# Optimization experiments

Hardware: AMD Instinct MI355X
Metric: run time of the kernel (lower is better)

Reference implementation:

```python
import jax, jax.numpy as jnp
import numpy as np

NUM_STATES = 8
HIDDEN_DIM = 1024
BATCH = 16384
DT = 0.01
PLANCK = 1.0
EPS_NORM = 1e-8
EPS_LOG = 1e-12


def setup_inputs() -> dict:
    key = jax.random.key(0)
    k1, k2, k3, k4, k5 = jax.random.split(key, 5)
    inv_sqrt_d = 1.0 / np.sqrt(HIDDEN_DIM)
    return {
        "input_state": jax.random.normal(k1, (BATCH, HIDDEN_DIM), dtype=jnp.float32),
        "amplitude_real": jax.random.normal(k2, (NUM_STATES, HIDDEN_DIM), dtype=jnp.float32) * inv_sqrt_d,
        "amplitude_imag": jax.random.normal(k3, (NUM_STATES, HIDDEN_DIM), dtype=jnp.float32) * inv_sqrt_d,
        "hamiltonian": jax.random.normal(k4, (NUM_STATES, NUM_STATES), dtype=jnp.float32) * 0.01,
        "projections": jax.random.normal(k5, (NUM_STATES, HIDDEN_DIM, HIDDEN_DIM), dtype=jnp.float32) * 0.01,
    }


def reference(input_state, amplitude_real, amplitude_imag, hamiltonian, projections):
    # complex amplitudes, normalized per state over hidden dim
    amps = amplitude_real + 1j * amplitude_imag  # [S, D] complex64
    norms = jnp.sum(jnp.abs(amps) ** 2, axis=1, keepdims=True)
    amps = amps / jnp.sqrt(norms + EPS_NORM)

    # unitary Hamiltonian evolution: expm(-i H dt / hbar) on the tiny SxS matrix
    H = (hamiltonian + hamiltonian.T) * 0.5
    U = jax.scipy.linalg.expm((-1j * DT / PLANCK) * H.astype(jnp.complex64))  # [S, S]
    amps = U @ amps  # [S, D]

    # decoherence at time_step=0: factor exp(0)=1, thermal noise scale 0 -> identity

    # superposed output: out[b,e] = sum_s Re(amps[s,e]) * (x @ P_s)[b,e]
    w = jnp.real(amps)  # [S, D]
    proj = jnp.einsum('bd,sde->bse', input_state, projections)  # [B, S, D]
    measured_output = jnp.einsum('bse,se->be', proj, w)  # [B, D]

    # measurement probabilities (computational basis)
    probs = jnp.abs(amps) ** 2
    probs = probs / (probs.sum(axis=0, keepdims=True) + EPS_NORM)
    collapse_prob = probs.mean(axis=1)  # [S]

    # metrics on rank-1 density matrix rho = outer(v, conj(v)), v = amps.flatten():
    # eigenvalues are {||v||^2, 0, ...} so the von Neumann entropy reduces to one term,
    # and sum|rho| = (sum|v|)^2, tr|diag| = sum|v|^2.
    v_abs = jnp.abs(amps.reshape(-1))
    lam = jnp.sum(v_abs ** 2)
    entanglement_entropy = -(lam * jnp.log(lam + EPS_LOG))
    coherence = jnp.sum(v_abs) ** 2 - lam

    amplitude_distribution = jnp.abs(amps) ** 2
    phase_evolution = jnp.angle(amps)

    return (measured_output, collapse_prob, entanglement_entropy, coherence,
            amplitude_distribution, phase_evolution)
```

## Files before the change

### kernel.cpp

```cpp
#include <hip/hip_runtime.h>
#include <hip/hip_bf16.h>

#define NSTATES 8
#define HD      1024
#define NBATCH  16384
#define NT      16

#define OUT_MEAS 0
#define OUT_CP   16777216
#define OUT_ENT  16777224
#define OUT_COH  16777225
#define OUT_AD   16777226
#define OUT_PH   16785418

typedef __attribute__((ext_vector_type(8))) short short8;
typedef __attribute__((ext_vector_type(4))) float f32x4;

__device__ __forceinline__ short f2bf(float f) {
    union { float f; unsigned u; } x; x.f = f;
    unsigned r = x.u + 0x7fffu + ((x.u >> 16) & 1u);
    return (short)(r >> 16);
}

__device__ __forceinline__ short8 pack8(float4 a, float4 b) {
    short8 v;
    v[0] = f2bf(a.x); v[1] = f2bf(a.y); v[2] = f2bf(a.z); v[3] = f2bf(a.w);
    v[4] = f2bf(b.x); v[5] = f2bf(b.y); v[6] = f2bf(b.z); v[7] = f2bf(b.w);
    return v;
}

__global__ __launch_bounds__(1024) void k_amps(const float* __restrict__ AR,
                                               const float* __restrict__ AI,
                                               const float* __restrict__ H,
                                               float* __restrict__ out,
                                               float* __restrict__ w) {
    __shared__ float redA[16 * NSTATES];
    __shared__ float redB[16 * 10];
    __shared__ float norms[NSTATES];
    __shared__ float sA[8][8], sA2[8][8], sA3[8][8];
    __shared__ float Ur[8][8], Ui[8][8];
    __shared__ float lamsa[2];

    const int tid = threadIdx.x;
    const int lane = tid & 63, wid = tid >> 6;
    const int d = tid;

    float arv[NSTATES], aiv[NSTATES];
    #pragma unroll
    for (int s = 0; s < NSTATES; s++) {
        arv[s] = AR[s * HD + d];
        aiv[s] = AI[s * HD + d];
    }
    float p[NSTATES];
    #pragma unroll
    for (int s = 0; s < NSTATES; s++) p[s] = arv[s] * arv[s] + aiv[s] * aiv[s];
    #pragma unroll
    for (int s = 0; s < NSTATES; s++)
        #pragma unroll
        for (int o = 32; o > 0; o >>= 1) p[s] += __shfl_down(p[s], o, 64);
    if (lane == 0)
        #pragma unroll
        for (int s = 0; s < NSTATES; s++) redA[wid * NSTATES + s] = p[s];
    if (tid < 64) {
        int i = tid >> 3, j = tid & 7;
        sA[i][j] = 0.5f * (H[i * 8 + j] + H[j * 8 + i]) * 0.01f;
    }
    __syncthreads();
    if (tid < 8) {
        float acc = 0.f;
        #pragma unroll
        for (int v = 0; v < 16; v++) acc += redA[v * NSTATES + tid];
        norms[tid] = acc;
    }
    if (tid < 64) {
        int i = tid >> 3, j = tid & 7;
        float acc = 0.f;
        #pragma unroll
        for (int k = 0; k < 8; k++) acc += sA[i][k] * sA[k][j];
        sA2[i][j] = acc;
    }
    __syncthreads();
    if (tid < 64) {
        int i = tid >> 3, j = tid & 7;
        float acc = 0.f;
        #pragma unroll
        for (int k = 0; k < 8; k++) acc += sA2[i][k] * sA[k][j];
        sA3[i][j] = acc;
        Ur[i][j] = ((i == j) ? 1.f : 0.f) - 0.5f * sA2[i][j];
        Ui[i][j] = -(sA[i][j] - sA3[i][j] * (1.f / 6.f));
    }
    __syncthreads();

    #pragma unroll
    for (int s = 0; s < NSTATES; s++) {
        float inv = 1.0f / sqrtf(norms[s] + 1e-8f);
        arv[s] *= inv;
        aiv[s] *= inv;
    }
    float nr[NSTATES], ni[NSTATES];
    #pragma unroll
    for (int s = 0; s < NSTATES; s++) {
        float xr = 0.f, xi = 0.f;
        #pragma unroll
        for (int t = 0; t < NSTATES; t++) {
            float ur = Ur[s][t], ui = Ui[s][t];
            xr += ur * arv[t] - ui * aiv[t];
            xi += ur * aiv[t] + ui * arv[t];
        }
        nr[s] = xr; ni[s] = xi;
    }
    float dist[NSTATES], csum = 0.f, sabs = 0.f;
    #pragma unroll
    for (int s = 0; s < NSTATES; s++) {
        dist[s] = nr[s] * nr[s] + ni[s] * ni[s];
        csum += dist[s];
        sabs += sqrtf(dist[s]);
    }
    #pragma unroll
    for (int s = 0; s < NSTATES; s++) {
        out[OUT_AD + s * HD + d] = dist[s];
        out[OUT_PH + s * HD + d] = atan2f(ni[s], nr[s]);
        w[s * HD + d] = nr[s];
    }
    float cinv = 1.0f / (csum + 1e-8f);
    float q[10];
    #pragma unroll
    for (int s = 0; s < NSTATES; s++) q[s] = dist[s] * cinv;
    q[8] = csum; q[9] = sabs;
    #pragma unroll
    for (int v = 0; v < 10; v++)
        #pragma unroll
        for (int o = 32; o > 0; o >>= 1) q[v] += __shfl_down(q[v], o, 64);
    if (lane == 0)
        #pragma unroll
        for (int v = 0; v < 10; v++) redB[wid * 10 + v] = q[v];
    __syncthreads();
    if (tid < 10) {
        float acc = 0.f;
        #pragma unroll
        for (int v = 0; v < 16; v++) acc += redB[v * 10 + tid];
        if (tid < 8)       out[OUT_CP + tid] = acc * (1.0f / HD);
        else               lamsa[tid - 8] = acc;
    }
    __syncthreads();
    if (tid == 0) {
        float lam = lamsa[0], sa = lamsa[1];
        out[OUT_ENT] = -(lam * logf(lam + 1e-12f));
        out[OUT_COH] = sa * sa - lam;
    }
}

__global__ __launch_bounds__(256) void k_pre(const float* __restrict__ X,
                                             short* __restrict__ Xb,
                                             const float* __restrict__ P,
                                             const float* __restrict__ w,
                                             short* __restrict__ Mt) {
    __shared__ float tile[64][65];
    if (blockIdx.x >= 256) {
        int idx = (blockIdx.x - 256) * 256 + threadIdx.x;
        const float* src = X + (size_t)idx * 8;
        float4 f0 = *reinterpret_cast<const float4*>(src);
        float4 f1 = *reinterpret_cast<const float4*>(src + 4);
        *reinterpret_cast<short8*>(Xb + (size_t)idx * 8) = pack8(f0, f1);
        return;
    }
    int d0 = (blockIdx.x >> 4) * 64;
    int e0 = (blockIdx.x & 15) * 64;
    int tx = threadIdx.x & 63, ty = threadIdx.x >> 6;
    float wv[NSTATES];
    #pragma unroll
    for (int s = 0; s < NSTATES; s++) wv[s] = w[s * HD + e0 + tx];
    #pragma unroll
    for (int j = 0; j < 16; j++) {
        int r = ty + 4 * j;
        float acc = 0.f;
        #pragma unroll
        for (int s = 0; s < NSTATES; s++)
            acc += wv[s] * P[(size_t)s * HD * HD + (size_t)(d0 + r) * HD + e0 + tx];
        tile[r][tx] = acc;
    }
    __syncthreads();
    #pragma unroll
    for (int j = 0; j < 16; j++) {
        int er = ty + 4 * j;
        Mt[(size_t)(e0 + er) * HD + d0 + tx] = f2bf(tile[tx][er]);
    }
}


__device__ __forceinline__ void stage_half(const short* __restrict__ srcBase,
                                           int rowbase, int h, int t2,
                                           short* dst, const int* goff,
                                           const int* ldsoff) {
    #pragma unroll
    for (int i = 0; i < 2; i++) {
        const short* g = srcBase + (size_t)(rowbase + h * 128) * HD + t2 * 64 + goff[i];
        __builtin_amdgcn_global_load_lds(
            (const __attribute__((address_space(1))) void*)g,
            (__attribute__((address_space(3))) void*)(dst + h * 8192 + ldsoff[i]),
            16, 0, 0);
    }
}

#define LOAD_A(qa)                                                             \
    _Pragma("unroll") for (int mf = 0; mf < 4; mf++)                           \
    _Pragma("unroll") for (int kk = 0; kk < 2; kk++)                           \
        af[mf][kk] = *reinterpret_cast<const short8*>(                         \
            &Acur[((qa) * 128 + wr64 + mf * 16 + ln15) * 64 + kx[kk]]);

#define LOAD_B_TO(dst, qb)                                                     \
    _Pragma("unroll") for (int nf = 0; nf < 2; nf++)                           \
    _Pragma("unroll") for (int kk = 0; kk < 2; kk++)                           \
        dst[nf][kk] = *reinterpret_cast<const short8*>(                        \
            &Bcur[((qb) * 128 + wn32 + nf * 16 + ln15) * 64 + kx[kk]]);

#define MFMA_P(qa, qb, breg)                                                   \
    _Pragma("unroll") for (int mf = 0; mf < 4; mf++)                           \
    _Pragma("unroll") for (int nf = 0; nf < 2; nf++)                           \
    _Pragma("unroll") for (int kk = 0; kk < 2; kk++)                           \
        acc[(qa) * 4 + mf][(qb) * 2 + nf] =                                    \
            __builtin_amdgcn_mfma_f32_16x16x32_bf16(                           \
                af[mf][kk], breg[nf][kk], acc[(qa) * 4 + mf][(qb) * 2 + nf], 0, 0, 0);

__global__ __launch_bounds__(512, 1) void k_gemm_8p(const short* __restrict__ Xb,
                                                    const short* __restrict__ Mt,
                                                    float* __restrict__ out) {
    __shared__ short As[2][256 * 64];
    __shared__ short Bs[2][256 * 64];

    const int bid = blockIdx.x;
    const int swz = (bid & 7) * 32 + (bid >> 3);
    const int brow = (swz >> 2) * 256;
    const int bcol = (swz & 3) * 256;

    const int tid  = threadIdx.x;
    const int lane = tid & 63, wid = tid >> 6;
    const int wr = wid >> 2, wn = wid & 3;
    const int ln15 = lane & 15, l16 = lane >> 4;
    const int wr64 = wr * 64;
    const int wn32 = wn * 32;

    int kx[2];
    kx[0] = ((l16 + 0) ^ (ln15 & 7)) * 8;
    kx[1] = ((l16 + 4) ^ (ln15 & 7)) * 8;

    int goff[2], ldsoff[2];
    #pragma unroll
    for (int i = 0; i < 2; i++) {
        int c = tid + 512 * i;
        int row = c >> 3, kc = c & 7;
        goff[i]   = row * HD + ((kc ^ (row & 7)) * 8);
        ldsoff[i] = c * 8;
    }

    short* A0 = &As[0][0]; short* A1b = &As[1][0];
    short* B0 = &Bs[0][0]; short* B1b = &Bs[1][0];

    f32x4 acc[8][4];
    #pragma unroll
    for (int m = 0; m < 8; m++)
        #pragma unroll
        for (int n = 0; n < 4; n++) acc[m][n] = (f32x4){0.f, 0.f, 0.f, 0.f};

    stage_half(Xb, brow, 0, 0, A0, goff, ldsoff);
    stage_half(Xb, brow, 1, 0, A0, goff, ldsoff);
    stage_half(Mt, bcol, 0, 0, B0, goff, ldsoff);
    stage_half(Mt, bcol, 1, 0, B0, goff, ldsoff);
    stage_half(Xb, brow, 0, 1, A1b, goff, ldsoff);
    stage_half(Mt, bcol, 1, 1, B1b, goff, ldsoff);
    asm volatile("s_waitcnt vmcnt(4)" ::: "memory");
    __builtin_amdgcn_s_barrier();

    short8 af[4][2], bfL[2][2], bfH[2][2];

    #pragma unroll 1
    for (int t = 0; t < NT; t++) {
        const int cur = t & 1;
        short* Acur  = cur ? A1b : A0;
        short* Bcur  = cur ? B1b : B0;
        short* Anext = cur ? A0 : A1b;
        short* Bnext = cur ? B0 : B1b;

        LOAD_A(0); LOAD_B_TO(bfL, 0);
        if (t + 1 < NT) stage_half(Xb, brow, 1, t + 1, Anext, goff, ldsoff);
        __builtin_amdgcn_s_barrier();
        __builtin_amdgcn_s_setprio(1);
        MFMA_P(0, 0, bfL);
        __builtin_amdgcn_s_setprio(0);

        LOAD_B_TO(bfH, 1);
        if (t + 1 < NT) stage_half(Mt, bcol, 0, t + 1, Bnext, goff, ldsoff);
        __builtin_amdgcn_s_barrier();
        __builtin_amdgcn_s_setprio(1);
        MFMA_P(0, 1, bfH);
        __builtin_amdgcn_s_setprio(0);

        LOAD_A(1);
        if (t + 2 < NT) stage_half(Xb, brow, 0, t + 2, Acur, goff, ldsoff);
        __builtin_amdgcn_s_barrier();
        __builtin_amdgcn_s_setprio(1);
        MFMA_P(1, 1, bfH);
        __builtin_amdgcn_s_setprio(0);

        if (t + 2 < NT) stage_half(Mt, bcol, 1, t + 2, Bcur, goff, ldsoff);
        __builtin_amdgcn_s_barrier();
        __builtin_amdgcn_s_setprio(1);
        MFMA_P(1, 0, bfL);
        __builtin_amdgcn_s_setprio(0);
        if (t + 2 < NT)      asm volatile("s_waitcnt vmcnt(4)" ::: "memory");
        else if (t + 1 < NT) asm volatile("s_waitcnt vmcnt(0)" ::: "memory");
        __builtin_amdgcn_s_barrier();
    }

    #pragma unroll
    for (int qa = 0; qa < 2; qa++)
        #pragma unroll
        for (int mf = 0; mf < 4; mf++)
            #pragma unroll
            for (int qb = 0; qb < 2; qb++)
                #pragma unroll
                for (int nf = 0; nf < 2; nf++)
                    #pragma unroll
                    for (int j = 0; j < 4; j++) {
                        int r = brow + qa * 128 + wr64 + mf * 16 + l16 * 4 + j;
                        int c = bcol + qb * 128 + wn32 + nf * 16 + ln15;
                        out[(size_t)r * HD + c] = acc[qa * 4 + mf][qb * 2 + nf][j];
                    }
}

extern "C" void kernel_launch(void* const* d_in, const int* in_sizes, int n_in,
                              void* d_out, int out_size, void* d_ws, size_t ws_size,
                              hipStream_t stream) {
    const float* X  = (const float*)d_in[0];
    const float* AR = (const float*)d_in[1];
    const float* AI = (const float*)d_in[2];
    const float* H  = (const float*)d_in[3];
    const float* P  = (const float*)d_in[4];
    float* out = (float*)d_out;

    char* ws = (char*)d_ws;
    float* w  = (float*)ws;
    short* Mt = (short*)(ws + 32768);
    short* Xb = (short*)(ws + 32768 + 2097152);

    k_amps<<<1, 1024, 0, stream>>>(AR, AI, H, out, w);
    k_pre<<<256 + (NBATCH * HD) / (256 * 8), 256, 0, stream>>>(X, Xb, P, w, Mt);
    k_gemm_8p<<<(NBATCH / 256) * (HD / 256), 512, 0, stream>>>(Xb, Mt, out);
}
```

Baseline: 76.50 us.

## Fuse fp32-to-bf16 conversion of X into GEMM A-tile staging

Removes the separate pass that converted the input activations to bf16 in workspace. The GEMM now loads fp32 X rows into registers, converts them with packed v_cvt_pk_bf16_f32 and writes them into LDS, prefetching one K-step ahead, while B tiles still use direct global-to-LDS loads. This avoids a full write and re-read of a bf16 copy of X, at the cost of reading fp32 X (twice the bytes) inside the GEMM, each X tile being re-read by the four column blocks, plus extra registers and a reworked barrier/waitcnt schedule. Rounding may differ slightly from the old software rounding for special values.

New measurement: 72.08 us. 5.8% less time.

```diff
diff --git a/kernel.cpp b/kernel.cpp
--- a/kernel.cpp
+++ b/kernel.cpp
@@ -22,11 +22,19 @@
     return (short)(r >> 16);
 }
 
-__device__ __forceinline__ short8 pack8(float4 a, float4 b) {
-    short8 v;
-    v[0] = f2bf(a.x); v[1] = f2bf(a.y); v[2] = f2bf(a.z); v[3] = f2bf(a.w);
-    v[4] = f2bf(b.x); v[5] = f2bf(b.y); v[6] = f2bf(b.z); v[7] = f2bf(b.w);
-    return v;
+__device__ __forceinline__ unsigned cvtpk(float lo, float hi) {
+    unsigned r;
+    asm("v_cvt_pk_bf16_f32 %0, %1, %2" : "=v"(r) : "v"(lo), "v"(hi));
+    return r;
+}
+
+__device__ __forceinline__ short8 pack8pk(float4 a, float4 b) {
+    union { unsigned u[4]; short8 s; } r;
+    r.u[0] = cvtpk(a.x, a.y);
+    r.u[1] = cvtpk(a.z, a.w);
+    r.u[2] = cvtpk(b.x, b.y);
+    r.u[3] = cvtpk(b.z, b.w);
+    return r.s;
 }
 
 __global__ __launch_bounds__(1024) void k_amps(const float* __restrict__ AR,
@@ -150,20 +158,10 @@
     }
 }
 
-__global__ __launch_bounds__(256) void k_pre(const float* __restrict__ X,
-                                             short* __restrict__ Xb,
-                                             const float* __restrict__ P,
-                                             const float* __restrict__ w,
-                                             short* __restrict__ Mt) {
+__global__ __launch_bounds__(256) void k_project_t(const float* __restrict__ P,
+                                                   const float* __restrict__ w,
+                                                   short* __restrict__ Mt) {
     __shared__ float tile[64][65];
-    if (blockIdx.x >= 256) {
-        int idx = (blockIdx.x - 256) * 256 + threadIdx.x;
-        const float* src = X + (size_t)idx * 8;
-        float4 f0 = *reinterpret_cast<const float4*>(src);
-        float4 f1 = *reinterpret_cast<const float4*>(src + 4);
-        *reinterpret_cast<short8*>(Xb + (size_t)idx * 8) = pack8(f0, f1);
-        return;
-    }
     int d0 = (blockIdx.x >> 4) * 64;
     int e0 = (blockIdx.x & 15) * 64;
     int tx = threadIdx.x & 63, ty = threadIdx.x >> 6;
@@ -188,10 +186,10 @@
 }
 
 
-__device__ __forceinline__ void stage_half(const short* __restrict__ srcBase,
-                                           int rowbase, int h, int t2,
-                                           short* dst, const int* goff,
-                                           const int* ldsoff) {
+__device__ __forceinline__ void stage_half_B(const short* __restrict__ srcBase,
+                                             int rowbase, int h, int t2,
+                                             short* dst, const int* goff,
+                                             const int* ldsoff) {
     #pragma unroll
     for (int i = 0; i < 2; i++) {
         const short* g = srcBase + (size_t)(rowbase + h * 128) * HD + t2 * 64 + goff[i];
@@ -201,6 +199,21 @@
             16, 0, 0);
     }
 }
+
+#define XLOAD(dst, h, t2)                                                      \
+    {                                                                          \
+        const float* b_ = X + (size_t)(brow + (h) * 128) * HD + (t2) * 64;     \
+        dst[0] = *reinterpret_cast<const float4*>(b_ + goff[0]);               \
+        dst[1] = *reinterpret_cast<const float4*>(b_ + goff[0] + 4);           \
+        dst[2] = *reinterpret_cast<const float4*>(b_ + goff[1]);               \
+        dst[3] = *reinterpret_cast<const float4*>(b_ + goff[1] + 4);           \
+    }
+
+#define XWRITE(dstlds, src)                                                    \
+    {                                                                          \
+        *reinterpret_cast<short8*>((dstlds) + ldsoff[0]) = pack8pk(src[0], src[1]); \
+        *reinterpret_cast<short8*>((dstlds) + ldsoff[1]) = pack8pk(src[2], src[3]); \
+    }
 
 #define LOAD_A(qa)                                                             \
     _Pragma("unroll") for (int mf = 0; mf < 4; mf++)                           \
@@ -222,9 +235,9 @@
             __builtin_amdgcn_mfma_f32_16x16x32_bf16(                           \
                 af[mf][kk], breg[nf][kk], acc[(qa) * 4 + mf][(qb) * 2 + nf], 0, 0, 0);
 
-__global__ __launch_bounds__(512, 1) void k_gemm_8p(const short* __restrict__ Xb,
-                                                    const short* __restrict__ Mt,
-                                                    float* __restrict__ out) {
+__global__ __launch_bounds__(512, 1) void k_gemm_jit(const float* __restrict__ X,
+                                                     const short* __restrict__ Mt,
+                                                     float* __restrict__ out) {
     __shared__ short As[2][256 * 64];
     __shared__ short Bs[2][256 * 64];
 
@@ -262,13 +275,16 @@
         #pragma unroll
         for (int n = 0; n < 4; n++) acc[m][n] = (f32x4){0.f, 0.f, 0.f, 0.f};
 
-    stage_half(Xb, brow, 0, 0, A0, goff, ldsoff);
-    stage_half(Xb, brow, 1, 0, A0, goff, ldsoff);
-    stage_half(Mt, bcol, 0, 0, B0, goff, ldsoff);
-    stage_half(Mt, bcol, 1, 0, B0, goff, ldsoff);
-    stage_half(Xb, brow, 0, 1, A1b, goff, ldsoff);
-    stage_half(Mt, bcol, 1, 1, B1b, goff, ldsoff);
-    asm volatile("s_waitcnt vmcnt(4)" ::: "memory");
+    float4 xrL[4], xrH[4];
+
+    XLOAD(xrL, 0, 0);
+    XLOAD(xrH, 1, 0);
+    stage_half_B(Mt, bcol, 0, 0, B0, goff, ldsoff);
+    stage_half_B(Mt, bcol, 1, 0, B0, goff, ldsoff);
+    stage_half_B(Mt, bcol, 1, 1, B1b, goff, ldsoff);
+    XWRITE(A0, xrL);
+    XWRITE(A0 + 8192, xrH);
+    asm volatile("s_waitcnt vmcnt(2) lgkmcnt(0)" ::: "memory");
     __builtin_amdgcn_s_barrier();
 
     short8 af[4][2], bfL[2][2], bfH[2][2];
@@ -282,34 +298,37 @@
         short* Bnext = cur ? B0 : B1b;
 
         LOAD_A(0); LOAD_B_TO(bfL, 0);
-        if (t + 1 < NT) stage_half(Xb, brow, 1, t + 1, Anext, goff, ldsoff);
+        if (t + 1 < NT) XLOAD(xrL, 0, (t + 1));
         __builtin_amdgcn_s_barrier();
         __builtin_amdgcn_s_setprio(1);
         MFMA_P(0, 0, bfL);
         __builtin_amdgcn_s_setprio(0);
 
         LOAD_B_TO(bfH, 1);
-        if (t + 1 < NT) stage_half(Mt, bcol, 0, t + 1, Bnext, goff, ldsoff);
+        if (t + 1 < NT) {
+            XLOAD(xrH, 1, (t + 1));
+            stage_half_B(Mt, bcol, 0, t + 1, Bnext, goff, ldsoff);
+        }
         __builtin_amdgcn_s_barrier();
         __builtin_amdgcn_s_setprio(1);
         MFMA_P(0, 1, bfH);
         __builtin_amdgcn_s_setprio(0);
 
         LOAD_A(1);
-        if (t + 2 < NT) stage_half(Xb, brow, 0, t + 2, Acur, goff, ldsoff);
+        if (t + 1 < NT) XWRITE(Anext, xrL);
         __builtin_amdgcn_s_barrier();
         __builtin_amdgcn_s_setprio(1);
         MFMA_P(1, 1, bfH);
         __builtin_amdgcn_s_setprio(0);
 
-        if (t + 2 < NT) stage_half(Mt, bcol, 1, t + 2, Bcur, goff, ldsoff);
+        if (t + 1 < NT) XWRITE(Anext + 8192, xrH);
+        if (t + 2 < NT) stage_half_B(Mt, bcol, 1, t + 2, Bcur, goff, ldsoff);
+        if (t + 2 < NT)      asm volatile("s_waitcnt vmcnt(2) lgkmcnt(0)" ::: "memory");
+        else if (t + 1 < NT) asm volatile("s_waitcnt vmcnt(0) lgkmcnt(0)" ::: "memory");
         __builtin_amdgcn_s_barrier();
         __builtin_amdgcn_s_setprio(1);
         MFMA_P(1, 0, bfL);
         __builtin_amdgcn_s_setprio(0);
-        if (t + 2 < NT)      asm volatile("s_waitcnt vmcnt(4)" ::: "memory");
-        else if (t + 1 < NT) asm volatile("s_waitcnt vmcnt(0)" ::: "memory");
-        __builtin_amdgcn_s_barrier();
     }
 
     #pragma unroll
@@ -341,9 +360,8 @@
     char* ws = (char*)d_ws;
     float* w  = (float*)ws;
     short* Mt = (short*)(ws + 32768);
-    short* Xb = (short*)(ws + 32768 + 2097152);
 
     k_amps<<<1, 1024, 0, stream>>>(AR, AI, H, out, w);
-    k_pre<<<256 + (NBATCH * HD) / (256 * 8), 256, 0, stream>>>(X, Xb, P, w, Mt);
-    k_gemm_8p<<<(NBATCH / 256) * (HD / 256), 512, 0, stream>>>(Xb, Mt, out);
-}
+    k_project_t<<<256, 256, 0, stream>>>(P, w, Mt);
+    k_gemm_jit<<<(NBATCH / 256) * (HD / 256), 512, 0, stream>>>(X, Mt, out);
+}
```

## Shrink GEMM block tile to 256x128 and drop one barrier per k-step

Applied to the files above, without the earlier changes.

The bf16 MFMA GEMM block tile narrows from 256x256 to 256x128, which doubles the grid to 512 blocks and halves the B-tile LDS buffers and accumulator registers. Each wave now owns one 16-wide N fragment per half, and B staging issues one global_load_lds per thread instead of two. The end-of-iteration vmcnt wait moves ahead of the last MFMA phase so it shares that phase's barrier, removing one barrier per k-step. The aim is better CU occupancy and load balance, with less register and LDS pressure. The cost is lower per-block data reuse, so the X tiles are read from memory twice as often.

Measured after the change: 83.56 us. +9.2%, slower.

```diff
diff --git a/kernel.cpp b/kernel.cpp
--- a/kernel.cpp
+++ b/kernel.cpp
@@ -188,10 +188,10 @@
 }
 
 
-__device__ __forceinline__ void stage_half(const short* __restrict__ srcBase,
-                                           int rowbase, int h, int t2,
-                                           short* dst, const int* goff,
-                                           const int* ldsoff) {
+__device__ __forceinline__ void stage_A(const short* __restrict__ srcBase,
+                                        int rowbase, int h, int t2,
+                                        short* dst, const int* goff,
+                                        const int* ldsoff) {
     #pragma unroll
     for (int i = 0; i < 2; i++) {
         const short* g = srcBase + (size_t)(rowbase + h * 128) * HD + t2 * 64 + goff[i];
@@ -202,6 +202,16 @@
     }
 }
 
+__device__ __forceinline__ void stage_B(const short* __restrict__ srcBase,
+                                        int colbase, int h, int t2,
+                                        short* dst, int goffB, int ldsoffB) {
+    const short* g = srcBase + (size_t)(colbase + h * 64) * HD + t2 * 64 + goffB;
+    __builtin_amdgcn_global_load_lds(
+        (const __attribute__((address_space(1))) void*)g,
+        (__attribute__((address_space(3))) void*)(dst + h * 4096 + ldsoffB),
+        16, 0, 0);
+}
+
 #define LOAD_A(qa)                                                             \
     _Pragma("unroll") for (int mf = 0; mf < 4; mf++)                           \
     _Pragma("unroll") for (int kk = 0; kk < 2; kk++)                           \
@@ -209,36 +219,34 @@
             &Acur[((qa) * 128 + wr64 + mf * 16 + ln15) * 64 + kx[kk]]);
 
 #define LOAD_B_TO(dst, qb)                                                     \
-    _Pragma("unroll") for (int nf = 0; nf < 2; nf++)                           \
     _Pragma("unroll") for (int kk = 0; kk < 2; kk++)                           \
-        dst[nf][kk] = *reinterpret_cast<const short8*>(                        \
-            &Bcur[((qb) * 128 + wn32 + nf * 16 + ln15) * 64 + kx[kk]]);
+        dst[kk] = *reinterpret_cast<const short8*>(                            \
+            &Bcur[((qb) * 64 + wn16 + ln15) * 64 + kx[kk]]);
 
 #define MFMA_P(qa, qb, breg)                                                   \
     _Pragma("unroll") for (int mf = 0; mf < 4; mf++)                           \
-    _Pragma("unroll") for (int nf = 0; nf < 2; nf++)                           \
     _Pragma("unroll") for (int kk = 0; kk < 2; kk++)                           \
-        acc[(qa) * 4 + mf][(qb) * 2 + nf] =                                    \
+        acc[(qa) * 4 + mf][(qb)] =                                             \
             __builtin_amdgcn_mfma_f32_16x16x32_bf16(                           \
-                af[mf][kk], breg[nf][kk], acc[(qa) * 4 + mf][(qb) * 2 + nf], 0, 0, 0);
-
-__global__ __launch_bounds__(512, 1) void k_gemm_8p(const short* __restrict__ Xb,
+                af[mf][kk], breg[kk], acc[(qa) * 4 + mf][(qb)], 0, 0, 0);
+
+__global__ __launch_bounds__(512, 1) void k_gemm_2r(const short* __restrict__ Xb,
                                                     const short* __restrict__ Mt,
                                                     float* __restrict__ out) {
     __shared__ short As[2][256 * 64];
-    __shared__ short Bs[2][256 * 64];
+    __shared__ short Bs[2][128 * 64];
 
     const int bid = blockIdx.x;
-    const int swz = (bid & 7) * 32 + (bid >> 3);
-    const int brow = (swz >> 2) * 256;
-    const int bcol = (swz & 3) * 256;
+    const int swz = (bid & 7) * 64 + (bid >> 3);
+    const int brow = (swz >> 3) * 256;
+    const int bcol = (swz & 7) * 128;
 
     const int tid  = threadIdx.x;
     const int lane = tid & 63, wid = tid >> 6;
     const int wr = wid >> 2, wn = wid & 3;
     const int ln15 = lane & 15, l16 = lane >> 4;
     const int wr64 = wr * 64;
-    const int wn32 = wn * 32;
+    const int wn16 = wn * 16;
 
     int kx[2];
     kx[0] = ((l16 + 0) ^ (ln15 & 7)) * 8;
@@ -252,26 +260,33 @@
         goff[i]   = row * HD + ((kc ^ (row & 7)) * 8);
         ldsoff[i] = c * 8;
     }
+    int goffB, ldsoffB;
+    {
+        int c = tid;
+        int row = c >> 3, kc = c & 7;
+        goffB   = row * HD + ((kc ^ (row & 7)) * 8);
+        ldsoffB = c * 8;
+    }
 
     short* A0 = &As[0][0]; short* A1b = &As[1][0];
     short* B0 = &Bs[0][0]; short* B1b = &Bs[1][0];
 
-    f32x4 acc[8][4];
+    f32x4 acc[8][2];
     #pragma unroll
     for (int m = 0; m < 8; m++)
         #pragma unroll
-        for (int n = 0; n < 4; n++) acc[m][n] = (f32x4){0.f, 0.f, 0.f, 0.f};
-
-    stage_half(Xb, brow, 0, 0, A0, goff, ldsoff);
-    stage_half(Xb, brow, 1, 0, A0, goff, ldsoff);
-    stage_half(Mt, bcol, 0, 0, B0, goff, ldsoff);
-    stage_half(Mt, bcol, 1, 0, B0, goff, ldsoff);
-    stage_half(Xb, brow, 0, 1, A1b, goff, ldsoff);
-    stage_half(Mt, bcol, 1, 1, B1b, goff, ldsoff);
-    asm volatile("s_waitcnt vmcnt(4)" ::: "memory");
+        for (int n = 0; n < 2; n++) acc[m][n] = (f32x4){0.f, 0.f, 0.f, 0.f};
+
+    stage_A(Xb, brow, 0, 0, A0, goff, ldsoff);
+    stage_A(Xb, brow, 1, 0, A0, goff, ldsoff);
+    stage_B(Mt, bcol, 0, 0, B0, goffB, ldsoffB);
+    stage_B(Mt, bcol, 1, 0, B0, goffB, ldsoffB);
+    stage_A(Xb, brow, 0, 1, A1b, goff, ldsoff);
+    stage_B(Mt, bcol, 1, 1, B1b, goffB, ldsoffB);
+    asm volatile("s_waitcnt vmcnt(3)" ::: "memory");
     __builtin_amdgcn_s_barrier();
 
-    short8 af[4][2], bfL[2][2], bfH[2][2];
+    short8 af[4][2], bfL[2], bfH[2];
 
     #pragma unroll 1
     for (int t = 0; t < NT; t++) {
@@ -282,34 +297,33 @@
         short* Bnext = cur ? B0 : B1b;
 
         LOAD_A(0); LOAD_B_TO(bfL, 0);
-        if (t + 1 < NT) stage_half(Xb, brow, 1, t + 1, Anext, goff, ldsoff);
+        if (t + 1 < NT) stage_A(Xb, brow, 1, t + 1, Anext, goff, ldsoff);
         __builtin_amdgcn_s_barrier();
         __builtin_amdgcn_s_setprio(1);
         MFMA_P(0, 0, bfL);
         __builtin_amdgcn_s_setprio(0);
 
         LOAD_B_TO(bfH, 1);
-        if (t + 1 < NT) stage_half(Mt, bcol, 0, t + 1, Bnext, goff, ldsoff);
+        if (t + 1 < NT) stage_B(Mt, bcol, 0, t + 1, Bnext, goffB, ldsoffB);
         __builtin_amdgcn_s_barrier();
         __builtin_amdgcn_s_setprio(1);
         MFMA_P(0, 1, bfH);
         __builtin_amdgcn_s_setprio(0);
 
         LOAD_A(1);
-        if (t + 2 < NT) stage_half(Xb, brow, 0, t + 2, Acur, goff, ldsoff);
+        if (t + 2 < NT) stage_A(Xb, brow, 0, t + 2, Acur, goff, ldsoff);
         __builtin_amdgcn_s_barrier();
         __builtin_amdgcn_s_setprio(1);
         MFMA_P(1, 1, bfH);
         __builtin_amdgcn_s_setprio(0);
 
-        if (t + 2 < NT) stage_half(Mt, bcol, 1, t + 2, Bcur, goff, ldsoff);
+        if (t + 2 < NT) stage_B(Mt, bcol, 1, t + 2, Bcur, goffB, ldsoffB);
+        if (t + 2 < NT)      asm volatile("s_waitcnt vmcnt(3)" ::: "memory");
+        else if (t + 1 < NT) asm volatile("s_waitcnt vmcnt(0)" ::: "memory");
         __builtin_amdgcn_s_barrier();
         __builtin_amdgcn_s_setprio(1);
         MFMA_P(1, 0, bfL);
         __builtin_amdgcn_s_setprio(0);
-        if (t + 2 < NT)      asm volatile("s_waitcnt vmcnt(4)" ::: "memory");
-        else if (t + 1 < NT) asm volatile("s_waitcnt vmcnt(0)" ::: "memory");
-        __builtin_amdgcn_s_barrier();
     }
 
     #pragma unroll
@@ -319,13 +333,11 @@
             #pragma unroll
             for (int qb = 0; qb < 2; qb++)
                 #pragma unroll
-                for (int nf = 0; nf < 2; nf++)
-                    #pragma unroll
-                    for (int j = 0; j < 4; j++) {
-                        int r = brow + qa * 128 + wr64 + mf * 16 + l16 * 4 + j;
-                        int c = bcol + qb * 128 + wn32 + nf * 16 + ln15;
-                        out[(size_t)r * HD + c] = acc[qa * 4 + mf][qb * 2 + nf][j];
-                    }
+                for (int j = 0; j < 4; j++) {
+                    int r = brow + qa * 128 + wr64 + mf * 16 + l16 * 4 + j;
+                    int c = bcol + qb * 64 + wn16 + ln15;
+                    out[(size_t)r * HD + c] = acc[qa * 4 + mf][qb][j];
+                }
 }
 
 extern "C" void kernel_launch(void* const* d_in, const int* in_sizes, int n_in,
@@ -345,5 +357,5 @@
 
     k_amps<<<1, 1024, 0, stream>>>(AR, AI, H, out, w);
     k_pre<<<256 + (NBATCH * HD) / (256 * 8), 256, 0, stream>>>(X, Xb, P, w, Mt);
-    k_gemm_8p<<<(NBATCH / 256) * (HD / 256), 512, 0, stream>>>(Xb, Mt, out);
-}
+    k_gemm_2r<<<(NBATCH / 256) * (HD / 128), 512, 0, stream>>>(Xb, Mt, out);
+}
```

## Fuse amplitude kernel into preprocessing kernel and merge GEMM loop barriers

Applied to the files above, without the earlier changes.

Removes the single-block k_amps launch. Each of the 256 projection blocks now recomputes the norms, the truncated unitary and its slice of weights, and one extra block writes the amplitude metrics. This drops a serialized launch and the workspace round-trip for w, at the cost of redundant small reductions in every projection block. In the GEMM main loop, the vmcnt wait moves before the preceding barrier, and the trailing barrier is removed so there is one fewer sync per iteration.

New measurement: 83.17 us. 1.09x slower.

```diff
diff --git a/kernel.cpp b/kernel.cpp
--- a/kernel.cpp
+++ b/kernel.cpp
@@ -29,161 +29,179 @@
     return v;
 }
 
-__global__ __launch_bounds__(1024) void k_amps(const float* __restrict__ AR,
-                                               const float* __restrict__ AI,
-                                               const float* __restrict__ H,
-                                               float* __restrict__ out,
-                                               float* __restrict__ w) {
-    __shared__ float redA[16 * NSTATES];
-    __shared__ float redB[16 * 10];
-    __shared__ float norms[NSTATES];
-    __shared__ float sA[8][8], sA2[8][8], sA3[8][8];
-    __shared__ float Ur[8][8], Ui[8][8];
-    __shared__ float lamsa[2];
-
+__global__ __launch_bounds__(256) void k_pre2(const float* __restrict__ X,
+                                              short* __restrict__ Xb,
+                                              const float* __restrict__ P,
+                                              const float* __restrict__ AR,
+                                              const float* __restrict__ AI,
+                                              const float* __restrict__ H,
+                                              short* __restrict__ Mt,
+                                              float* __restrict__ out) {
+    const int bid = blockIdx.x;
     const int tid = threadIdx.x;
-    const int lane = tid & 63, wid = tid >> 6;
-    const int d = tid;
-
-    float arv[NSTATES], aiv[NSTATES];
-    #pragma unroll
-    for (int s = 0; s < NSTATES; s++) {
-        arv[s] = AR[s * HD + d];
-        aiv[s] = AI[s * HD + d];
-    }
-    float p[NSTATES];
-    #pragma unroll
-    for (int s = 0; s < NSTATES; s++) p[s] = arv[s] * arv[s] + aiv[s] * aiv[s];
-    #pragma unroll
-    for (int s = 0; s < NSTATES; s++)
-        #pragma unroll
-        for (int o = 32; o > 0; o >>= 1) p[s] += __shfl_down(p[s], o, 64);
-    if (lane == 0)
-        #pragma unroll
-        for (int s = 0; s < NSTATES; s++) redA[wid * NSTATES + s] = p[s];
-    if (tid < 64) {
-        int i = tid >> 3, j = tid & 7;
-        sA[i][j] = 0.5f * (H[i * 8 + j] + H[j * 8 + i]) * 0.01f;
-    }
-    __syncthreads();
-    if (tid < 8) {
-        float acc = 0.f;
-        #pragma unroll
-        for (int v = 0; v < 16; v++) acc += redA[v * NSTATES + tid];
-        norms[tid] = acc;
-    }
-    if (tid < 64) {
-        int i = tid >> 3, j = tid & 7;
-        float acc = 0.f;
-        #pragma unroll
-        for (int k = 0; k < 8; k++) acc += sA[i][k] * sA[k][j];
-        sA2[i][j] = acc;
-    }
-    __syncthreads();
-    if (tid < 64) {
-        int i = tid >> 3, j = tid & 7;
-        float acc = 0.f;
-        #pragma unroll
-        for (int k = 0; k < 8; k++) acc += sA2[i][k] * sA[k][j];
-        sA3[i][j] = acc;
-        Ur[i][j] = ((i == j) ? 1.f : 0.f) - 0.5f * sA2[i][j];
-        Ui[i][j] = -(sA[i][j] - sA3[i][j] * (1.f / 6.f));
-    }
-    __syncthreads();
-
-    #pragma unroll
-    for (int s = 0; s < NSTATES; s++) {
-        float inv = 1.0f / sqrtf(norms[s] + 1e-8f);
-        arv[s] *= inv;
-        aiv[s] *= inv;
-    }
-    float nr[NSTATES], ni[NSTATES];
-    #pragma unroll
-    for (int s = 0; s < NSTATES; s++) {
-        float xr = 0.f, xi = 0.f;
-        #pragma unroll
-        for (int t = 0; t < NSTATES; t++) {
-            float ur = Ur[s][t], ui = Ui[s][t];
-            xr += ur * arv[t] - ui * aiv[t];
-            xi += ur * aiv[t] + ui * arv[t];
-        }
-        nr[s] = xr; ni[s] = xi;
-    }
-    float dist[NSTATES], csum = 0.f, sabs = 0.f;
-    #pragma unroll
-    for (int s = 0; s < NSTATES; s++) {
-        dist[s] = nr[s] * nr[s] + ni[s] * ni[s];
-        csum += dist[s];
-        sabs += sqrtf(dist[s]);
-    }
-    #pragma unroll
-    for (int s = 0; s < NSTATES; s++) {
-        out[OUT_AD + s * HD + d] = dist[s];
-        out[OUT_PH + s * HD + d] = atan2f(ni[s], nr[s]);
-        w[s * HD + d] = nr[s];
-    }
-    float cinv = 1.0f / (csum + 1e-8f);
-    float q[10];
-    #pragma unroll
-    for (int s = 0; s < NSTATES; s++) q[s] = dist[s] * cinv;
-    q[8] = csum; q[9] = sabs;
-    #pragma unroll
-    for (int v = 0; v < 10; v++)
-        #pragma unroll
-        for (int o = 32; o > 0; o >>= 1) q[v] += __shfl_down(q[v], o, 64);
-    if (lane == 0)
-        #pragma unroll
-        for (int v = 0; v < 10; v++) redB[wid * 10 + v] = q[v];
-    __syncthreads();
-    if (tid < 10) {
-        float acc = 0.f;
-        #pragma unroll
-        for (int v = 0; v < 16; v++) acc += redB[v * 10 + tid];
-        if (tid < 8)       out[OUT_CP + tid] = acc * (1.0f / HD);
-        else               lamsa[tid - 8] = acc;
-    }
-    __syncthreads();
-    if (tid == 0) {
-        float lam = lamsa[0], sa = lamsa[1];
-        out[OUT_ENT] = -(lam * logf(lam + 1e-12f));
-        out[OUT_COH] = sa * sa - lam;
-    }
-}
-
-__global__ __launch_bounds__(256) void k_pre(const float* __restrict__ X,
-                                             short* __restrict__ Xb,
-                                             const float* __restrict__ P,
-                                             const float* __restrict__ w,
-                                             short* __restrict__ Mt) {
-    __shared__ float tile[64][65];
-    if (blockIdx.x >= 256) {
-        int idx = (blockIdx.x - 256) * 256 + threadIdx.x;
+
+    if (bid >= 256 && bid < 256 + 8192) {
+        int idx = (bid - 256) * 256 + tid;
         const float* src = X + (size_t)idx * 8;
         float4 f0 = *reinterpret_cast<const float4*>(src);
         float4 f1 = *reinterpret_cast<const float4*>(src + 4);
         *reinterpret_cast<short8*>(Xb + (size_t)idx * 8) = pack8(f0, f1);
         return;
     }
-    int d0 = (blockIdx.x >> 4) * 64;
-    int e0 = (blockIdx.x & 15) * 64;
-    int tx = threadIdx.x & 63, ty = threadIdx.x >> 6;
-    float wv[NSTATES];
-    #pragma unroll
-    for (int s = 0; s < NSTATES; s++) wv[s] = w[s * HD + e0 + tx];
-    #pragma unroll
-    for (int j = 0; j < 16; j++) {
-        int r = ty + 4 * j;
+
+    __shared__ float redN[4][NSTATES];
+    __shared__ float norms[NSTATES];
+    __shared__ float sA[8][8], sA2[8][8];
+    __shared__ float Ur[8][8], Ui[8][8];
+    __shared__ float tile[64][65];
+    __shared__ float redC[4][10];
+    __shared__ float lamsa[2];
+
+    const int lane = tid & 63, wid = tid >> 6;
+
+    float p[NSTATES];
+    #pragma unroll
+    for (int s = 0; s < NSTATES; s++) p[s] = 0.f;
+    #pragma unroll
+    for (int c = 0; c < 4; c++) {
+        int d = tid + c * 256;
+        #pragma unroll
+        for (int s = 0; s < NSTATES; s++) {
+            float a = AR[s * HD + d], b = AI[s * HD + d];
+            p[s] += a * a + b * b;
+        }
+    }
+    #pragma unroll
+    for (int s = 0; s < NSTATES; s++)
+        #pragma unroll
+        for (int o = 32; o > 0; o >>= 1) p[s] += __shfl_down(p[s], o, 64);
+    if (lane == 0)
+        #pragma unroll
+        for (int s = 0; s < NSTATES; s++) redN[wid][s] = p[s];
+    if (tid < 64) {
+        int i = tid >> 3, j = tid & 7;
+        sA[i][j] = 0.5f * (H[i * 8 + j] + H[j * 8 + i]) * 0.01f;
+    }
+    __syncthreads();
+    if (tid < 8)
+        norms[tid] = redN[0][tid] + redN[1][tid] + redN[2][tid] + redN[3][tid];
+    if (tid < 64) {
+        int i = tid >> 3, j = tid & 7;
         float acc = 0.f;
         #pragma unroll
-        for (int s = 0; s < NSTATES; s++)
-            acc += wv[s] * P[(size_t)s * HD * HD + (size_t)(d0 + r) * HD + e0 + tx];
-        tile[r][tx] = acc;
-    }
-    __syncthreads();
-    #pragma unroll
-    for (int j = 0; j < 16; j++) {
-        int er = ty + 4 * j;
-        Mt[(size_t)(e0 + er) * HD + d0 + tx] = f2bf(tile[tx][er]);
+        for (int k = 0; k < 8; k++) acc += sA[i][k] * sA[k][j];
+        sA2[i][j] = acc;
+    }
+    __syncthreads();
+    if (tid < 64) {
+        int i = tid >> 3, j = tid & 7;
+        float a3 = 0.f;
+        #pragma unroll
+        for (int k = 0; k < 8; k++) a3 += sA2[i][k] * sA[k][j];
+        Ur[i][j] = ((i == j) ? 1.f : 0.f) - 0.5f * sA2[i][j];
+        Ui[i][j] = -(sA[i][j] - a3 * (1.f / 6.f));
+    }
+    __syncthreads();
+
+    if (bid < 256) {
+        int d0 = (bid >> 4) * 64;
+        int e0 = (bid & 15) * 64;
+        int tx = tid & 63, ty = tid >> 6;
+        float inv[NSTATES], arv[NSTATES], aiv[NSTATES], wv[NSTATES];
+        #pragma unroll
+        for (int s = 0; s < NSTATES; s++) inv[s] = 1.0f / sqrtf(norms[s] + 1e-8f);
+        #pragma unroll
+        for (int s = 0; s < NSTATES; s++) {
+            arv[s] = AR[s * HD + e0 + tx] * inv[s];
+            aiv[s] = AI[s * HD + e0 + tx] * inv[s];
+        }
+        #pragma unroll
+        for (int s = 0; s < NSTATES; s++) {
+            float xr = 0.f;
+            #pragma unroll
+            for (int t = 0; t < NSTATES; t++)
+                xr += Ur[s][t] * arv[t] - Ui[s][t] * aiv[t];
+            wv[s] = xr;
+        }
+        #pragma unroll
+        for (int j = 0; j < 16; j++) {
+            int r = ty + 4 * j;
+            float acc = 0.f;
+            #pragma unroll
+            for (int s = 0; s < NSTATES; s++)
+                acc += wv[s] * P[(size_t)s * HD * HD + (size_t)(d0 + r) * HD + e0 + tx];
+            tile[r][tx] = acc;
+        }
+        __syncthreads();
+        #pragma unroll
+        for (int j = 0; j < 16; j++) {
+            int er = ty + 4 * j;
+            Mt[(size_t)(e0 + er) * HD + d0 + tx] = f2bf(tile[tx][er]);
+        }
+        return;
+    }
+
+    float inv[NSTATES];
+    #pragma unroll
+    for (int s = 0; s < NSTATES; s++) inv[s] = 1.0f / sqrtf(norms[s] + 1e-8f);
+    float q[10];
+    #pragma unroll
+    for (int v = 0; v < 10; v++) q[v] = 0.f;
+    #pragma unroll
+    for (int c = 0; c < 4; c++) {
+        int d = tid + c * 256;
+        float arv[NSTATES], aiv[NSTATES], nr[NSTATES], ni[NSTATES];
+        #pragma unroll
+        for (int s = 0; s < NSTATES; s++) {
+            arv[s] = AR[s * HD + d] * inv[s];
+            aiv[s] = AI[s * HD + d] * inv[s];
+        }
+        #pragma unroll
+        for (int s = 0; s < NSTATES; s++) {
+            float xr = 0.f, xi = 0.f;
+            #pragma unroll
+            for (int t = 0; t < NSTATES; t++) {
+                float ur = Ur[s][t], ui = Ui[s][t];
+                xr += ur * arv[t] - ui * aiv[t];
+                xi += ur * aiv[t] + ui * arv[t];
+            }
+            nr[s] = xr; ni[s] = xi;
+        }
+        float dist[NSTATES], csum = 0.f, sabs = 0.f;
+        #pragma unroll
+        for (int s = 0; s < NSTATES; s++) {
+            dist[s] = nr[s] * nr[s] + ni[s] * ni[s];
+            csum += dist[s];
+            sabs += sqrtf(dist[s]);
+        }
+        #pragma unroll
+        for (int s = 0; s < NSTATES; s++) {
+            out[OUT_AD + s * HD + d] = dist[s];
+            out[OUT_PH + s * HD + d] = atan2f(ni[s], nr[s]);
+        }
+        float cinv = 1.0f / (csum + 1e-8f);
+        #pragma unroll
+        for (int s = 0; s < NSTATES; s++) q[s] += dist[s] * cinv;
+        q[8] += csum; q[9] += sabs;
+    }
+    #pragma unroll
+    for (int v = 0; v < 10; v++)
+        #pragma unroll
+        for (int o = 32; o > 0; o >>= 1) q[v] += __shfl_down(q[v], o, 64);
+    if (lane == 0)
+        #pragma unroll
+        for (int v = 0; v < 10; v++) redC[wid][v] = q[v];
+    __syncthreads();
+    if (tid < 10) {
+        float acc = redC[0][tid] + redC[1][tid] + redC[2][tid] + redC[3][tid];
+        if (tid < 8)       out[OUT_CP + tid] = acc * (1.0f / HD);
+        else               lamsa[tid - 8] = acc;
+    }
+    __syncthreads();
+    if (tid == 0) {
+        float lam = lamsa[0], sa = lamsa[1];
+        out[OUT_ENT] = -(lam * logf(lam + 1e-12f));
+        out[OUT_COH] = sa * sa - lam;
     }
 }
 
@@ -303,13 +321,12 @@
         __builtin_amdgcn_s_setprio(0);
 
         if (t + 2 < NT) stage_half(Mt, bcol, 1, t + 2, Bcur, goff, ldsoff);
+        if (t + 2 < NT)      asm volatile("s_waitcnt vmcnt(4)" ::: "memory");
+        else if (t + 1 < NT) asm volatile("s_waitcnt vmcnt(0)" ::: "memory");
         __builtin_amdgcn_s_barrier();
         __builtin_amdgcn_s_setprio(1);
         MFMA_P(1, 0, bfL);
         __builtin_amdgcn_s_setprio(0);
-        if (t + 2 < NT)      asm volatile("s_waitcnt vmcnt(4)" ::: "memory");
-        else if (t + 1 < NT) asm volatile("s_waitcnt vmcnt(0)" ::: "memory");
-        __builtin_amdgcn_s_barrier();
     }
 
     #pragma unroll
@@ -339,11 +356,9 @@
     float* out = (float*)d_out;
 
     char* ws = (char*)d_ws;
-    float* w  = (float*)ws;
-    short* Mt = (short*)(ws + 32768);
-    short* Xb = (short*)(ws + 32768 + 2097152);
-
-    k_amps<<<1, 1024, 0, stream>>>(AR, AI, H, out, w);
-    k_pre<<<256 + (NBATCH * HD) / (256 * 8), 256, 0, stream>>>(X, Xb, P, w, Mt);
+    short* Mt = (short*)ws;
+    short* Xb = (short*)(ws + 2097152);
+
+    k_pre2<<<256 + 8192 + 1, 256, 0, stream>>>(X, Xb, P, AR, AI, H, Mt, out);
     k_gemm_8p<<<(NBATCH / 256) * (HD / 256), 512, 0, stream>>>(Xb, Mt, out);
 }
```
